# Optimization experiments

Measured on AMD Instinct MI355X. Metric: run time of the kernel, lower is better.

Reference implementation:

```python
import jax, jax.numpy as jnp
import numpy as np

B, D, E, K, H = 4096, 1024, 8, 2, 8  # batch, dim, num_experts, top_k, num_heads


def setup_inputs() -> dict:
    key = jax.random.key(0)
    ks = jax.random.split(key, 6)
    w = lambda k, shape: jax.random.normal(k, shape, jnp.float32) * 0.02
    return dict(
        x=jax.random.normal(ks[0], (B, D), jnp.float32),
        y=jax.random.normal(ks[1], (B, D), jnp.float32),
        Wqkv=w(ks[2], (E, D, 3 * D)),      # per-expert qkv weight (no bias)
        Wg=w(ks[3], (D, E)),               # gating weight
        bg=jnp.zeros((E,), jnp.float32),   # gating bias
        Wp=w(ks[4], (D, D)),               # output proj weight
        bp=jnp.zeros((D,), jnp.float32),   # output proj bias
        expert_bias=jnp.zeros((E,), jnp.float32),  # non-trainable load-balance bias
    )


def reference(x, y, Wqkv, Wg, bg, Wp, bp, expert_bias):
    Bn, Dn = x.shape
    hd = Dn // H
    scale = hd ** -0.5

    # gating: softmax then add (non-trainable) expert bias, then top-k
    gate = jax.nn.softmax(x @ Wg + bg, axis=-1) + expert_bias          # [B,E]
    vals, idx = jax.lax.top_k(gate, K)                                  # [B,K]
    # combine top-k gate values into a per-expert weight vector (indices distinct)
    g = jnp.sum(jax.nn.one_hot(idx, E, dtype=x.dtype) * vals[..., None], axis=1)  # [B,E]

    # dense per-expert qkv projections, then gate-weighted combine
    qkv_x = jnp.einsum('be,beh->bh', g, jnp.einsum('bd,edh->beh', x, Wqkv))  # [B,3D]
    qkv_y = jnp.einsum('be,beh->bh', g, jnp.einsum('bd,edh->beh', y, Wqkv))  # [B,3D]

    qkv_x = qkv_x.reshape(Bn, 3, H, hd)
    qkv_y = qkv_y.reshape(Bn, 3, H, hd)
    q = qkv_y[:, 0]   # [B,H,hd] (query from y)
    k = qkv_x[:, 1]   # [B,H,hd]
    v = qkv_x[:, 2]   # [B,H,hd]

    # attention across the heads axis (heads act as the sequence here)
    attn = jax.nn.softmax(jnp.einsum('bid,bjd->bij', q, k) * scale, axis=-1)  # [B,H,H]
    out = jnp.einsum('bij,bjd->bid', attn, v)                                 # [B,H,hd]
    # torch: .transpose(1,2).reshape(B,N) -> flatten as (hd, H)
    out = jnp.swapaxes(out, 1, 2).reshape(Bn, Dn)
    return out @ Wp + bp
```

## Files before the change

### kernel.cpp

```cpp
#include <hip/hip_runtime.h>
#include <cstdint>
#include <cstddef>

#define B_TOK 4096
#define D_DIM 1024
#define E_NUM 8
#define N3    3072

typedef float f32x4 __attribute__((ext_vector_type(4)));
typedef __bf16 bf16x8 __attribute__((ext_vector_type(8)));

__device__ __forceinline__ unsigned short f2bf(float f) {
  unsigned u = __float_as_uint(f);
  u += 0x7fffu + ((u >> 16) & 1u);
  return (unsigned short)(u >> 16);
}
__device__ __forceinline__ float bf_lo(unsigned u) { return __uint_as_float(u << 16); }
__device__ __forceinline__ float bf_hi(unsigned u) { return __uint_as_float(u & 0xffff0000u); }

__device__ __forceinline__ void stage16(const unsigned short* g, unsigned short* lds) {
  __builtin_amdgcn_global_load_lds(
      (const __attribute__((address_space(1))) void*)(uintptr_t)(const void*)g,
      (__attribute__((address_space(3))) void*)(uintptr_t)(void*)lds,
      16, 0, 0);
}

#define PREP_B   B_TOK
#define TQ_B     (16 * 48 * 8)
#define TP_B     (16 * 16)
#define FUSED_B  (PREP_B + TQ_B + TP_B)

__global__ __launch_bounds__(256)
void fused_prep_kernel(const float* __restrict__ x, const float* __restrict__ y,
                       const float* __restrict__ Wg, const float* __restrict__ bg,
                       const float* __restrict__ ebias,
                       const float* __restrict__ Wqkv, const float* __restrict__ Wp,
                       unsigned short* __restrict__ xb, unsigned short* __restrict__ yb,
                       unsigned short* __restrict__ wqkvT, unsigned short* __restrict__ wpT,
                       int* __restrict__ tok_expert, float* __restrict__ tok_weight)
{
  __shared__ float tile[64][65];
  __shared__ float red[4][E_NUM];
  const int t = threadIdx.x;
  const int grp = blockIdx.x / 41;
  const int pos = blockIdx.x % 41;

  if (pos < 16) {
    const int b = grp * 16 + pos;
    const int w = t >> 6, l = t & 63;
    float4 xv = *(const float4*)(x + (size_t)b * D_DIM + 4 * t);
    float4 yv = *(const float4*)(y + (size_t)b * D_DIM + 4 * t);
    ushort4 px; px.x = f2bf(xv.x); px.y = f2bf(xv.y); px.z = f2bf(xv.z); px.w = f2bf(xv.w);
    *(ushort4*)(xb + (size_t)b * D_DIM + 4 * t) = px;
    ushort4 py; py.x = f2bf(yv.x); py.y = f2bf(yv.y); py.z = f2bf(yv.z); py.w = f2bf(yv.w);
    *(ushort4*)(yb + (size_t)b * D_DIM + 4 * t) = py;

    float a[E_NUM];
#pragma unroll
    for (int e = 0; e < E_NUM; ++e) a[e] = 0.f;
    const float xa[4] = {xv.x, xv.y, xv.z, xv.w};
#pragma unroll
    for (int j = 0; j < 4; ++j) {
      const float4* wr4 = (const float4*)(Wg + (size_t)(4 * t + j) * E_NUM);
      float4 w0 = wr4[0], w1 = wr4[1];
      a[0] += xa[j] * w0.x; a[1] += xa[j] * w0.y;
      a[2] += xa[j] * w0.z; a[3] += xa[j] * w0.w;
      a[4] += xa[j] * w1.x; a[5] += xa[j] * w1.y;
      a[6] += xa[j] * w1.z; a[7] += xa[j] * w1.w;
    }

    float s0, s1, s2, s3;
    {
      const bool b0 = (l & 1);
      float r0_ = __shfl_xor(b0 ? a[0] : a[4], 1);
      float r1_ = __shfl_xor(b0 ? a[1] : a[5], 1);
      float r2_ = __shfl_xor(b0 ? a[2] : a[6], 1);
      float r3_ = __shfl_xor(b0 ? a[3] : a[7], 1);
      s0 = (b0 ? a[4] : a[0]) + r0_;
      s1 = (b0 ? a[5] : a[1]) + r1_;
      s2 = (b0 ? a[6] : a[2]) + r2_;
      s3 = (b0 ? a[7] : a[3]) + r3_;
    }
    float u0, u1;
    {
      const bool b1 = (l & 2);
      float r0_ = __shfl_xor(b1 ? s0 : s2, 2);
      float r1_ = __shfl_xor(b1 ? s1 : s3, 2);
      u0 = (b1 ? s2 : s0) + r0_;
      u1 = (b1 ? s3 : s1) + r1_;
    }
    float v_;
    {
      const bool b2 = (l & 4);
      float r0_ = __shfl_xor(b2 ? u0 : u1, 4);
      v_ = (b2 ? u1 : u0) + r0_;
    }
    v_ += __shfl_xor(v_, 8);
    v_ += __shfl_xor(v_, 16);
    v_ += __shfl_xor(v_, 32);
    if (l < 8) {
      const int e = ((l & 1) << 2) | (l & 2) | ((l >> 2) & 1);
      red[w][e] = v_;
    }
    __syncthreads();
    if (t == 0) {
      float logit[E_NUM];
#pragma unroll
      for (int e = 0; e < E_NUM; ++e)
        logit[e] = red[0][e] + red[1][e] + red[2][e] + red[3][e] + bg[e];
      float m = logit[0];
#pragma unroll
      for (int e = 1; e < E_NUM; ++e) m = fmaxf(m, logit[e]);
      float p[E_NUM], s = 0.f;
#pragma unroll
      for (int e = 0; e < E_NUM; ++e) { p[e] = expf(logit[e] - m); s += p[e]; }
      float inv = 1.f / s;
      float gate[E_NUM];
#pragma unroll
      for (int e = 0; e < E_NUM; ++e) gate[e] = p[e] * inv + ebias[e];
      int i1 = 0; float v1 = gate[0];
#pragma unroll
      for (int e = 1; e < E_NUM; ++e) if (gate[e] > v1) { v1 = gate[e]; i1 = e; }
      int i2 = -1; float v2 = -1e30f;
#pragma unroll
      for (int e = 0; e < E_NUM; ++e) if (e != i1 && gate[e] > v2) { v2 = gate[e]; i2 = e; }
      tok_expert[b * 2] = i1; tok_expert[b * 2 + 1] = i2;
      tok_weight[b * 2] = v1; tok_weight[b * 2 + 1] = v2;
    }
    return;
  }

  const int tid2 = grp * 25 + (pos - 16);
  const float* in; unsigned short* outp; int R, C, r0, c0; size_t mo;
  if (tid2 < TQ_B) {
    int id = tid2;
    int rt = id & 15; int rest = id >> 4;
    int ct = rest % 48; int mz = rest / 48;
    in = Wqkv; outp = wqkvT; R = 1024; C = 3072;
    r0 = rt * 64; c0 = ct * 64; mo = (size_t)mz * R * C;
  } else {
    int id = tid2 - TQ_B;
    int rt = id & 15; int ct = id >> 4;
    in = Wp; outp = wpT; R = 1024; C = 1024;
    r0 = rt * 64; c0 = ct * 64; mo = 0;
  }
  const int tq = t & 15;
  const int tr = t >> 4;
  {
    const float* src = in + mo + (size_t)(r0 + tr) * C + (c0 + 4 * tq);
    float4 v0 = *(const float4*)(src);
    float4 v1 = *(const float4*)(src + (size_t)16 * C);
    float4 v2 = *(const float4*)(src + (size_t)32 * C);
    float4 v3 = *(const float4*)(src + (size_t)48 * C);
    tile[tr][4 * tq] = v0.x;      tile[tr][4 * tq + 1] = v0.y;
    tile[tr][4 * tq + 2] = v0.z;  tile[tr][4 * tq + 3] = v0.w;
    tile[tr + 16][4 * tq] = v1.x;     tile[tr + 16][4 * tq + 1] = v1.y;
    tile[tr + 16][4 * tq + 2] = v1.z; tile[tr + 16][4 * tq + 3] = v1.w;
    tile[tr + 32][4 * tq] = v2.x;     tile[tr + 32][4 * tq + 1] = v2.y;
    tile[tr + 32][4 * tq + 2] = v2.z; tile[tr + 32][4 * tq + 3] = v2.w;
    tile[tr + 48][4 * tq] = v3.x;     tile[tr + 48][4 * tq + 1] = v3.y;
    tile[tr + 48][4 * tq + 2] = v3.z; tile[tr + 48][4 * tq + 3] = v3.w;
  }
  __syncthreads();
  {
    const int rw = 4 * tq;
#pragma unroll
    for (int p = 0; p < 4; ++p) {
      const int c = tr + 16 * p;
      float a0 = tile[rw][c], a1 = tile[rw + 1][c];
      float a2 = tile[rw + 2][c], a3 = tile[rw + 3][c];
      ushort4 o;
      o.x = f2bf(a0); o.y = f2bf(a1); o.z = f2bf(a2); o.w = f2bf(a3);
      *(ushort4*)(outp + mo + (size_t)(c0 + c) * R + (r0 + rw)) = o;
    }
  }
}

#define NT_ENT (B_TOK * 2)
#define ENT_PER_T (NT_ENT / 256)
__global__ __launch_bounds__(256)
void route_kernel(const int* __restrict__ tok_expert, const float* __restrict__ tok_weight,
                  int* __restrict__ eoff, int* __restrict__ slot_token,
                  float* __restrict__ slot_weight, int* __restrict__ tok_slot)
{
  __shared__ int cnt[256][E_NUM];
  __shared__ int sub[E_NUM][8];
  __shared__ int tot[E_NUM];
  __shared__ int eoff_s[E_NUM];
  const int t = threadIdx.x;

  {
    int h[E_NUM];
#pragma unroll
    for (int e = 0; e < E_NUM; ++e) h[e] = 0;
    for (int p = 0; p < ENT_PER_T; ++p) {
      int e = tok_expert[t * ENT_PER_T + p];
      h[e]++;
    }
#pragma unroll
    for (int e = 0; e < E_NUM; ++e) cnt[t][e] = h[e];
  }
  __syncthreads();

  if (t < 64) {
    int e = t & 7, g = t >> 3;
    int run = 0;
    for (int i = g * 32; i < (g + 1) * 32; ++i) {
      int v = cnt[i][e];
      cnt[i][e] = run;
      run += v;
    }
    sub[e][g] = run;
  }
  __syncthreads();
  if (t < E_NUM) {
    int run = 0;
#pragma unroll
    for (int g = 0; g < 8; ++g) {
      int v = sub[t][g];
      sub[t][g] = run;
      run += v;
    }
    tot[t] = run;
  }
  __syncthreads();
  if (t < 64) {
    int e = t & 7, g = t >> 3;
    int basev = sub[e][g];
    for (int i = g * 32; i < (g + 1) * 32; ++i) cnt[i][e] += basev;
  }
  if (t == 0) {
    int a = 0;
#pragma unroll
    for (int e = 0; e < E_NUM; ++e) { eoff_s[e] = a; eoff[e] = a; a += tot[e]; }
    eoff[E_NUM] = a;
  }
  __syncthreads();

  for (int p = 0; p < ENT_PER_T; ++p) {
    int i = t * ENT_PER_T + p;
    int e = tok_expert[i];
    int sl = eoff_s[e] + cnt[t][e];
    cnt[t][e] = cnt[t][e] + 1;
    slot_token[sl] = i >> 1;
    slot_weight[sl] = tok_weight[i];
    tok_slot[i] = sl;
  }
}

#define MOE_NWG 6144
#define MOE_CPX (MOE_NWG / 8)
__global__ __launch_bounds__(256, 4)
void moe_gemm_kernel(const unsigned short* __restrict__ yb, const unsigned short* __restrict__ xb,
                     const unsigned short* __restrict__ wqkvT,
                     unsigned short* __restrict__ qkvslot,
                     const int* __restrict__ slot_token, const float* __restrict__ slot_weight,
                     const int* __restrict__ eoff)
{
  __shared__ __align__(16) unsigned short As[128 * 64];
  __shared__ __align__(16) unsigned short Bs[128 * 64];

  const int id = blockIdx.x;
  const int swz = (id & 7) * MOE_CPX + (id >> 3);
  const int nt = swz % 24;
  const int mtE = swz / 24;
  const int mt = mtE & 31;
  const int e  = mtE >> 5;

  const int tid = threadIdx.x;
  const int w = tid >> 6, l = tid & 63;
  const int base = eoff[e], cnt = eoff[e + 1] - base;
  if (mt * 128 >= cnt) return;
  const int slot_base = base + mt * 128;
  const int valid = min(128, cnt - mt * 128);
  const int nc = nt * 128;

  const unsigned short* Abase = (nt < 8) ? yb : xb;
  const unsigned short* Bbase = wqkvT + ((size_t)e * N3 + nc) * D_DIM;

  const int csw = (((l & 7) ^ (l >> 3)) << 3);
  const unsigned short* aptr[4];
  const unsigned short* bptr[4];
#pragma unroll
  for (int i = 0; i < 4; ++i) {
    int r = (w * 4 + i) * 8 + (l >> 3);
    int rA = r < valid ? r : (valid - 1);
    int t = slot_token[slot_base + rA];
    aptr[i] = Abase + (size_t)t * D_DIM + csw;
    bptr[i] = Bbase + (size_t)r * D_DIM + csw;
  }

  f32x4 acc[4][4];
#pragma unroll
  for (int mi = 0; mi < 4; ++mi)
#pragma unroll
    for (int ni = 0; ni < 4; ++ni) acc[mi][ni] = (f32x4){0.f, 0.f, 0.f, 0.f};

  const int wr = w >> 1, wc = w & 1;
  const int arow = wr * 64 + (l & 15);
  const int brow = wc * 64 + (l & 15);

  for (int kt = 0; kt < 16; ++kt) {
    __syncthreads();
#pragma unroll
    for (int i = 0; i < 4; ++i) {
      stage16(aptr[i] + kt * 64, &As[(w * 4 + i) * 512]);
      stage16(bptr[i] + kt * 64, &Bs[(w * 4 + i) * 512]);
    }
    __syncthreads();
#pragma unroll
    for (int ks = 0; ks < 2; ++ks) {
      const int eoffk = (((ks * 4 + (l >> 4)) ^ (l & 7)) << 3);
      bf16x8 af[4], bfv[4];
#pragma unroll
      for (int mi = 0; mi < 4; ++mi)
        af[mi] = *(const bf16x8*)&As[(arow + mi * 16) * 64 + eoffk];
#pragma unroll
      for (int ni = 0; ni < 4; ++ni)
        bfv[ni] = *(const bf16x8*)&Bs[(brow + ni * 16) * 64 + eoffk];
#pragma unroll
      for (int mi = 0; mi < 4; ++mi)
#pragma unroll
        for (int ni = 0; ni < 4; ++ni)
          acc[mi][ni] = __builtin_amdgcn_mfma_f32_16x16x32_bf16(af[mi], bfv[ni], acc[mi][ni], 0, 0, 0);
    }
  }

  const int crow0 = wr * 64 + ((l >> 4) << 2);
  const int ccol = wc * 64 + (l & 15);
#pragma unroll
  for (int mi = 0; mi < 4; ++mi) {
#pragma unroll
    for (int j = 0; j < 4; ++j) {
      int rloc = crow0 + mi * 16 + j;
      if (rloc < valid) {
        int sl = slot_base + rloc;
        float wgt = slot_weight[sl];
        size_t ro = (size_t)sl * N3 + nc + ccol;
#pragma unroll
        for (int ni = 0; ni < 4; ++ni)
          qkvslot[ro + ni * 16] = f2bf(acc[mi][ni][j] * wgt);
      }
    }
  }
}

__global__ __launch_bounds__(256)
void attn_kernel(const unsigned short* __restrict__ qkvslot,
                 const int* __restrict__ tok_slot,
                 unsigned short* __restrict__ attno)
{
  __shared__ unsigned short obuf[4][1024];
  const int w = threadIdx.x >> 6, l = threadIdx.x & 63;
  const int b0 = blockIdx.x * 4;
  const int b = b0 + w;
  const int s0 = tok_slot[b * 2], s1 = tok_slot[b * 2 + 1];
  const unsigned* p0 = (const unsigned*)(qkvslot + (size_t)s0 * N3);
  const unsigned* p1 = (const unsigned*)(qkvslot + (size_t)s1 * N3);

  float q[8][2], k[8][2], v[8][2];
#pragma unroll
  for (int i = 0; i < 8; ++i) {
    unsigned a0 = p0[i * 64 + l],        a1 = p1[i * 64 + l];
    unsigned b0v = p0[512 + i * 64 + l], b1v = p1[512 + i * 64 + l];
    unsigned c0 = p0[1024 + i * 64 + l], c1 = p1[1024 + i * 64 + l];
    q[i][0] = bf_lo(a0) + bf_lo(a1); q[i][1] = bf_hi(a0) + bf_hi(a1);
    k[i][0] = bf_lo(b0v) + bf_lo(b1v); k[i][1] = bf_hi(b0v) + bf_hi(b1v);
    v[i][0] = bf_lo(c0) + bf_lo(c1); v[i][1] = bf_hi(c0) + bf_hi(c1);
  }

  float S[8][8];
#pragma unroll
  for (int i = 0; i < 8; ++i)
#pragma unroll
    for (int j = 0; j < 8; ++j)
      S[i][j] = q[i][0] * k[j][0] + q[i][1] * k[j][1];

#pragma unroll
  for (int off = 32; off; off >>= 1)
#pragma unroll
    for (int i = 0; i < 8; ++i)
#pragma unroll
      for (int j = 0; j < 8; ++j)
        S[i][j] += __shfl_xor(S[i][j], off);

  const float scale = 0.08838834764831843f;
#pragma unroll
  for (int i = 0; i < 8; ++i) {
    float m = S[i][0];
#pragma unroll
    for (int j = 1; j < 8; ++j) m = fmaxf(m, S[i][j]);
    float P[8], sum = 0.f;
#pragma unroll
    for (int j = 0; j < 8; ++j) { P[j] = expf((S[i][j] - m) * scale); sum += P[j]; }
    float inv = 1.f / sum;
    float o0 = 0.f, o1 = 0.f;
#pragma unroll
    for (int j = 0; j < 8; ++j) { o0 += P[j] * v[j][0]; o1 += P[j] * v[j][1]; }
    obuf[w][(2 * l) * 8 + i]     = f2bf(o0 * inv);
    obuf[w][(2 * l + 1) * 8 + i] = f2bf(o1 * inv);
  }
  __syncthreads();
  const int t = threadIdx.x;
#pragma unroll
  for (int p = 0; p < 4; ++p) {
    int j = t + 256 * p;
    int tk = j >> 8, c = j & 255;
    *(ushort4*)(attno + (size_t)(b0 + tk) * D_DIM + 4 * c) = *(ushort4*)&obuf[tk][4 * c];
  }
}

__global__ __launch_bounds__(256, 4)
void final_gemm_kernel(const unsigned short* __restrict__ attno,
                       const unsigned short* __restrict__ wpT,
                       const float* __restrict__ bp,
                       float* __restrict__ out)
{
  __shared__ __align__(16) unsigned short As[64 * 64];
  __shared__ __align__(16) unsigned short Bs[128 * 64];

  const int tid = threadIdx.x;
  const int w = tid >> 6, l = tid & 63;
  const int nt = blockIdx.x, mt = blockIdx.y;

  const int csw = (((l & 7) ^ (l >> 3)) << 3);
  const unsigned short* aptr[2];
  const unsigned short* bptr[4];
#pragma unroll
  for (int i = 0; i < 2; ++i) {
    int r = (w * 2 + i) * 8 + (l >> 3);
    aptr[i] = attno + (size_t)(mt * 64 + r) * D_DIM + csw;
  }
#pragma unroll
  for (int i = 0; i < 4; ++i) {
    int r = (w * 4 + i) * 8 + (l >> 3);
    bptr[i] = wpT + (size_t)(nt * 128 + r) * D_DIM + csw;
  }

  f32x4 acc[2][4];
#pragma unroll
  for (int mi = 0; mi < 2; ++mi)
#pragma unroll
    for (int ni = 0; ni < 4; ++ni) acc[mi][ni] = (f32x4){0.f, 0.f, 0.f, 0.f};

  const int wr = w >> 1, wc = w & 1;
  const int arow = wr * 32 + (l & 15);
  const int brow = wc * 64 + (l & 15);

  for (int kt = 0; kt < 16; ++kt) {
    __syncthreads();
#pragma unroll
    for (int i = 0; i < 2; ++i)
      stage16(aptr[i] + kt * 64, &As[(w * 2 + i) * 512]);
#pragma unroll
    for (int i = 0; i < 4; ++i)
      stage16(bptr[i] + kt * 64, &Bs[(w * 4 + i) * 512]);
    __syncthreads();
#pragma unroll
    for (int ks = 0; ks < 2; ++ks) {
      const int eoffk = (((ks * 4 + (l >> 4)) ^ (l & 7)) << 3);
      bf16x8 af[2], bfv[4];
#pragma unroll
      for (int mi = 0; mi < 2; ++mi)
        af[mi] = *(const bf16x8*)&As[(arow + mi * 16) * 64 + eoffk];
#pragma unroll
      for (int ni = 0; ni < 4; ++ni)
        bfv[ni] = *(const bf16x8*)&Bs[(brow + ni * 16) * 64 + eoffk];
#pragma unroll
      for (int mi = 0; mi < 2; ++mi)
#pragma unroll
        for (int ni = 0; ni < 4; ++ni)
          acc[mi][ni] = __builtin_amdgcn_mfma_f32_16x16x32_bf16(af[mi], bfv[ni], acc[mi][ni], 0, 0, 0);
    }
  }

  const int crow0 = wr * 32 + ((l >> 4) << 2);
  const int ccol = wc * 64 + (l & 15);
#pragma unroll
  for (int mi = 0; mi < 2; ++mi) {
#pragma unroll
    for (int j = 0; j < 4; ++j) {
      int rg = mt * 64 + crow0 + mi * 16 + j;
#pragma unroll
      for (int ni = 0; ni < 4; ++ni) {
        int cg = nt * 128 + ccol + ni * 16;
        out[(size_t)rg * D_DIM + cg] = acc[mi][ni][j] + bp[cg];
      }
    }
  }
}

extern "C" void kernel_launch(void* const* d_in, const int* in_sizes, int n_in,
                              void* d_out, int out_size, void* d_ws, size_t ws_size,
                              hipStream_t stream)
{
  const float* x     = (const float*)d_in[0];
  const float* y     = (const float*)d_in[1];
  const float* Wqkv  = (const float*)d_in[2];
  const float* Wg    = (const float*)d_in[3];
  const float* bg    = (const float*)d_in[4];
  const float* Wp    = (const float*)d_in[5];
  const float* bp    = (const float*)d_in[6];
  const float* ebias = (const float*)d_in[7];
  float* out = (float*)d_out;

  char* ws = (char*)d_ws;
  size_t off_b = 0;
  auto take = [&](size_t bytes) -> char* {
    char* p = ws + off_b;
    off_b += (bytes + 255) & ~(size_t)255;
    return p;
  };
  unsigned short* xb       = (unsigned short*)take((size_t)B_TOK * D_DIM * 2);
  unsigned short* yb       = (unsigned short*)take((size_t)B_TOK * D_DIM * 2);
  unsigned short* wqkvT    = (unsigned short*)take((size_t)E_NUM * N3 * D_DIM * 2);
  unsigned short* wpT      = (unsigned short*)take((size_t)D_DIM * D_DIM * 2);
  unsigned short* qkvslot  = (unsigned short*)take((size_t)B_TOK * 2 * N3 * 2);
  unsigned short* attno    = (unsigned short*)take((size_t)B_TOK * D_DIM * 2);
  int*   eoff        = (int*)take(16 * 4);
  int*   tok_expert  = (int*)take((size_t)B_TOK * 2 * 4);
  float* tok_weight  = (float*)take((size_t)B_TOK * 2 * 4);
  int*   tok_slot    = (int*)take((size_t)B_TOK * 2 * 4);
  int*   slot_token  = (int*)take((size_t)B_TOK * 2 * 4);
  float* slot_weight = (float*)take((size_t)B_TOK * 2 * 4);

  if (ws_size < off_b) return;

  fused_prep_kernel<<<FUSED_B, 256, 0, stream>>>(x, y, Wg, bg, ebias, Wqkv, Wp,
                                                 xb, yb, wqkvT, wpT, tok_expert, tok_weight);
  route_kernel<<<1, 256, 0, stream>>>(tok_expert, tok_weight, eoff, slot_token,
                                      slot_weight, tok_slot);
  moe_gemm_kernel<<<MOE_NWG, 256, 0, stream>>>(yb, xb, wqkvT, qkvslot,
                                               slot_token, slot_weight, eoff);
  attn_kernel<<<B_TOK / 4, 256, 0, stream>>>(qkvslot, tok_slot, attno);
  final_gemm_kernel<<<dim3(8, 64), 256, 0, stream>>>(attno, wpT, bp, out);
}
```

Measured before the change: 161.5 us.

## Fold routing into prep kernel via last-block counter and compact MoE tile grid

Removes the separate single-block route kernel by having the last finishing gating block (tracked by an atomic done-counter) perform the expert histogram, prefix sum and slot scatter inside the prep kernel. That block also emits a compact list of valid (expert, m-tile) pairs, so the MoE GEMM launches 24*71 workgroups instead of 6144, most of which previously exited immediately. This saves one launch and the cost of scheduling many empty workgroups. In exchange it adds a memset launch, an atomic plus threadfence in every gating block, and a serialized tail in the last block.

```diff
diff --git a/kernel.cpp b/kernel.cpp
--- a/kernel.cpp
+++ b/kernel.cpp
@@ -29,6 +29,9 @@
 #define TQ_B     (16 * 48 * 8)
 #define TP_B     (16 * 16)
 #define FUSED_B  (PREP_B + TQ_B + TP_B)
+
+#define NT_ENT (B_TOK * 2)
+#define ENT_PER_T (NT_ENT / 256)
 
 __global__ __launch_bounds__(256)
 void fused_prep_kernel(const float* __restrict__ x, const float* __restrict__ y,
@@ -37,10 +40,20 @@
                        const float* __restrict__ Wqkv, const float* __restrict__ Wp,
                        unsigned short* __restrict__ xb, unsigned short* __restrict__ yb,
                        unsigned short* __restrict__ wqkvT, unsigned short* __restrict__ wpT,
-                       int* __restrict__ tok_expert, float* __restrict__ tok_weight)
+                       int* __restrict__ tok_expert, float* __restrict__ tok_weight,
+                       int* __restrict__ done_ctr,
+                       int* __restrict__ eoff, int* __restrict__ slot_token,
+                       float* __restrict__ slot_weight, int* __restrict__ tok_slot,
+                       int* __restrict__ tile_list, int* __restrict__ n_tiles)
 {
   __shared__ float tile[64][65];
   __shared__ float red[4][E_NUM];
+  __shared__ int last_s;
+  int (*rcnt)[E_NUM] = (int (*)[E_NUM])&tile[0][0];
+  int (*rsub)[8]     = (int (*)[8])((char*)&tile[0][0] + 8192);
+  int* rtot          = (int*)((char*)&tile[0][0] + 8448);
+  int* reoff         = (int*)((char*)&tile[0][0] + 8480);
+
   const int t = threadIdx.x;
   const int grp = blockIdx.x / 41;
   const int pos = blockIdx.x % 41;
@@ -126,6 +139,74 @@
       for (int e = 0; e < E_NUM; ++e) if (e != i1 && gate[e] > v2) { v2 = gate[e]; i2 = e; }
       tok_expert[b * 2] = i1; tok_expert[b * 2 + 1] = i2;
       tok_weight[b * 2] = v1; tok_weight[b * 2 + 1] = v2;
+      __threadfence();
+      int old = atomicAdd(done_ctr, 1);
+      last_s = (old == PREP_B - 1);
+    }
+    __syncthreads();
+    if (!last_s) return;
+    __threadfence();
+
+    {
+      int h[E_NUM];
+#pragma unroll
+      for (int e = 0; e < E_NUM; ++e) h[e] = 0;
+      for (int p = 0; p < ENT_PER_T; ++p) {
+        int e = tok_expert[t * ENT_PER_T + p];
+        h[e]++;
+      }
+#pragma unroll
+      for (int e = 0; e < E_NUM; ++e) rcnt[t][e] = h[e];
+    }
+    __syncthreads();
+    if (t < 64) {
+      int e = t & 7, g = t >> 3;
+      int run = 0;
+      for (int i = g * 32; i < (g + 1) * 32; ++i) {
+        int v = rcnt[i][e];
+        rcnt[i][e] = run;
+        run += v;
+      }
+      rsub[e][g] = run;
+    }
+    __syncthreads();
+    if (t < E_NUM) {
+      int run = 0;
+#pragma unroll
+      for (int g = 0; g < 8; ++g) {
+        int v = rsub[t][g];
+        rsub[t][g] = run;
+        run += v;
+      }
+      rtot[t] = run;
+    }
+    __syncthreads();
+    if (t < 64) {
+      int e = t & 7, g = t >> 3;
+      int basev = rsub[e][g];
+      for (int i = g * 32; i < (g + 1) * 32; ++i) rcnt[i][e] += basev;
+    }
+    if (t == 0) {
+      int a = 0, n = 0;
+#pragma unroll
+      for (int e = 0; e < E_NUM; ++e) {
+        reoff[e] = a; eoff[e] = a;
+        int c = rtot[e];
+        for (int j = 0; j * 128 < c; ++j) tile_list[n++] = e | (j << 8);
+        a += c;
+      }
+      eoff[E_NUM] = a;
+      n_tiles[0] = n;
+    }
+    __syncthreads();
+    for (int p = 0; p < ENT_PER_T; ++p) {
+      int i = t * ENT_PER_T + p;
+      int e = tok_expert[i];
+      int sl = reoff[e] + rcnt[t][e];
+      rcnt[t][e] = rcnt[t][e] + 1;
+      slot_token[sl] = i >> 1;
+      slot_weight[sl] = tok_weight[i];
+      tok_slot[i] = sl;
     }
     return;
   }
@@ -176,101 +257,32 @@
   }
 }
 
-#define NT_ENT (B_TOK * 2)
-#define ENT_PER_T (NT_ENT / 256)
-__global__ __launch_bounds__(256)
-void route_kernel(const int* __restrict__ tok_expert, const float* __restrict__ tok_weight,
-                  int* __restrict__ eoff, int* __restrict__ slot_token,
-                  float* __restrict__ slot_weight, int* __restrict__ tok_slot)
-{
-  __shared__ int cnt[256][E_NUM];
-  __shared__ int sub[E_NUM][8];
-  __shared__ int tot[E_NUM];
-  __shared__ int eoff_s[E_NUM];
-  const int t = threadIdx.x;
-
-  {
-    int h[E_NUM];
-#pragma unroll
-    for (int e = 0; e < E_NUM; ++e) h[e] = 0;
-    for (int p = 0; p < ENT_PER_T; ++p) {
-      int e = tok_expert[t * ENT_PER_T + p];
-      h[e]++;
-    }
-#pragma unroll
-    for (int e = 0; e < E_NUM; ++e) cnt[t][e] = h[e];
-  }
-  __syncthreads();
-
-  if (t < 64) {
-    int e = t & 7, g = t >> 3;
-    int run = 0;
-    for (int i = g * 32; i < (g + 1) * 32; ++i) {
-      int v = cnt[i][e];
-      cnt[i][e] = run;
-      run += v;
-    }
-    sub[e][g] = run;
-  }
-  __syncthreads();
-  if (t < E_NUM) {
-    int run = 0;
-#pragma unroll
-    for (int g = 0; g < 8; ++g) {
-      int v = sub[t][g];
-      sub[t][g] = run;
-      run += v;
-    }
-    tot[t] = run;
-  }
-  __syncthreads();
-  if (t < 64) {
-    int e = t & 7, g = t >> 3;
-    int basev = sub[e][g];
-    for (int i = g * 32; i < (g + 1) * 32; ++i) cnt[i][e] += basev;
-  }
-  if (t == 0) {
-    int a = 0;
-#pragma unroll
-    for (int e = 0; e < E_NUM; ++e) { eoff_s[e] = a; eoff[e] = a; a += tot[e]; }
-    eoff[E_NUM] = a;
-  }
-  __syncthreads();
-
-  for (int p = 0; p < ENT_PER_T; ++p) {
-    int i = t * ENT_PER_T + p;
-    int e = tok_expert[i];
-    int sl = eoff_s[e] + cnt[t][e];
-    cnt[t][e] = cnt[t][e] + 1;
-    slot_token[sl] = i >> 1;
-    slot_weight[sl] = tok_weight[i];
-    tok_slot[i] = sl;
-  }
-}
-
-#define MOE_NWG 6144
-#define MOE_CPX (MOE_NWG / 8)
+#define MOE_MAXT 71
+#define MOE_NWG  (24 * MOE_MAXT)
+#define MOE_CPX  (MOE_NWG / 8)
 __global__ __launch_bounds__(256, 4)
 void moe_gemm_kernel(const unsigned short* __restrict__ yb, const unsigned short* __restrict__ xb,
                      const unsigned short* __restrict__ wqkvT,
                      unsigned short* __restrict__ qkvslot,
                      const int* __restrict__ slot_token, const float* __restrict__ slot_weight,
-                     const int* __restrict__ eoff)
+                     const int* __restrict__ eoff,
+                     const int* __restrict__ tile_list, const int* __restrict__ n_tiles)
 {
   __shared__ __align__(16) unsigned short As[128 * 64];
   __shared__ __align__(16) unsigned short Bs[128 * 64];
 
   const int id = blockIdx.x;
   const int swz = (id & 7) * MOE_CPX + (id >> 3);
-  const int nt = swz % 24;
-  const int mtE = swz / 24;
-  const int mt = mtE & 31;
-  const int e  = mtE >> 5;
+  const int tix = swz / 24;
+  const int nt  = swz % 24;
+  if (tix >= n_tiles[0]) return;
+  const int packed = tile_list[tix];
+  const int e  = packed & 255;
+  const int mt = packed >> 8;
 
   const int tid = threadIdx.x;
   const int w = tid >> 6, l = tid & 63;
   const int base = eoff[e], cnt = eoff[e + 1] - base;
-  if (mt * 128 >= cnt) return;
   const int slot_base = base + mt * 128;
   const int valid = min(128, cnt - mt * 128);
   const int nc = nt * 128;
@@ -523,15 +535,21 @@
   int*   tok_slot    = (int*)take((size_t)B_TOK * 2 * 4);
   int*   slot_token  = (int*)take((size_t)B_TOK * 2 * 4);
   float* slot_weight = (float*)take((size_t)B_TOK * 2 * 4);
+  int*   done_ctr    = (int*)take(4);
+  int*   tile_list   = (int*)take(MOE_MAXT * 4);
+  int*   n_tiles     = (int*)take(4);
 
   if (ws_size < off_b) return;
 
+  hipMemsetAsync(done_ctr, 0, 4, stream);
+
   fused_prep_kernel<<<FUSED_B, 256, 0, stream>>>(x, y, Wg, bg, ebias, Wqkv, Wp,
-                                                 xb, yb, wqkvT, wpT, tok_expert, tok_weight);
-  route_kernel<<<1, 256, 0, stream>>>(tok_expert, tok_weight, eoff, slot_token,
-                                      slot_weight, tok_slot);
+                                                 xb, yb, wqkvT, wpT, tok_expert, tok_weight,
+                                                 done_ctr, eoff, slot_token, slot_weight,
+                                                 tok_slot, tile_list, n_tiles);
   moe_gemm_kernel<<<MOE_NWG, 256, 0, stream>>>(yb, xb, wqkvT, qkvslot,
-                                               slot_token, slot_weight, eoff);
+                                               slot_token, slot_weight, eoff,
+                                               tile_list, n_tiles);
   attn_kernel<<<B_TOK / 4, 256, 0, stream>>>(qkvslot, tok_slot, attno);
   final_gemm_kernel<<<dim3(8, 64), 256, 0, stream>>>(attno, wpT, bp, out);
 }
```

Result: slower. 366.6 us (+127.1%).

## Double-buffer LDS staging in MoE GEMM with prefetch two K-tiles ahead

Applied to the files above, without the earlier changes.

Switches the MoE GEMM's A and B shared-memory tiles to two buffers and prefetches two K-steps ahead with global_load_lds, waiting with explicit vmcnt counts instead of full syncthreads. This lets global-to-LDS loads overlap the MFMA work rather than stalling each iteration. LDS use doubles to 64KB per block, which may cut occupancy below the launch-bounds target of 4 blocks. The hand-written waitcnt values also depend on the exact number of outstanding loads.

```diff
diff --git a/kernel.cpp b/kernel.cpp
--- a/kernel.cpp
+++ b/kernel.cpp
@@ -257,8 +257,8 @@
                      const int* __restrict__ slot_token, const float* __restrict__ slot_weight,
                      const int* __restrict__ eoff)
 {
-  __shared__ __align__(16) unsigned short As[128 * 64];
-  __shared__ __align__(16) unsigned short Bs[128 * 64];
+  __shared__ __align__(16) unsigned short As[2][128 * 64];
+  __shared__ __align__(16) unsigned short Bs[2][128 * 64];
 
   const int id = blockIdx.x;
   const int swz = (id & 7) * MOE_CPX + (id >> 3);
@@ -300,29 +300,50 @@
   const int arow = wr * 64 + (l & 15);
   const int brow = wc * 64 + (l & 15);
 
+#pragma unroll
+  for (int i = 0; i < 4; ++i) {
+    stage16(aptr[i], &As[0][(w * 4 + i) * 512]);
+    stage16(bptr[i], &Bs[0][(w * 4 + i) * 512]);
+  }
+#pragma unroll
+  for (int i = 0; i < 4; ++i) {
+    stage16(aptr[i] + 64, &As[1][(w * 4 + i) * 512]);
+    stage16(bptr[i] + 64, &Bs[1][(w * 4 + i) * 512]);
+  }
+
   for (int kt = 0; kt < 16; ++kt) {
-    __syncthreads();
-#pragma unroll
-    for (int i = 0; i < 4; ++i) {
-      stage16(aptr[i] + kt * 64, &As[(w * 4 + i) * 512]);
-      stage16(bptr[i] + kt * 64, &Bs[(w * 4 + i) * 512]);
-    }
-    __syncthreads();
+    if (kt < 15) asm volatile("s_waitcnt vmcnt(8)" ::: "memory");
+    else         asm volatile("s_waitcnt vmcnt(0)" ::: "memory");
+    __builtin_amdgcn_s_barrier();
+    __builtin_amdgcn_sched_barrier(0);
+
+    const unsigned short* Asc = As[kt & 1];
+    const unsigned short* Bsc = Bs[kt & 1];
 #pragma unroll
     for (int ks = 0; ks < 2; ++ks) {
       const int eoffk = (((ks * 4 + (l >> 4)) ^ (l & 7)) << 3);
       bf16x8 af[4], bfv[4];
 #pragma unroll
       for (int mi = 0; mi < 4; ++mi)
-        af[mi] = *(const bf16x8*)&As[(arow + mi * 16) * 64 + eoffk];
+        af[mi] = *(const bf16x8*)&Asc[(arow + mi * 16) * 64 + eoffk];
 #pragma unroll
       for (int ni = 0; ni < 4; ++ni)
-        bfv[ni] = *(const bf16x8*)&Bs[(brow + ni * 16) * 64 + eoffk];
+        bfv[ni] = *(const bf16x8*)&Bsc[(brow + ni * 16) * 64 + eoffk];
 #pragma unroll
       for (int mi = 0; mi < 4; ++mi)
 #pragma unroll
         for (int ni = 0; ni < 4; ++ni)
           acc[mi][ni] = __builtin_amdgcn_mfma_f32_16x16x32_bf16(af[mi], bfv[ni], acc[mi][ni], 0, 0, 0);
+    }
+
+    __builtin_amdgcn_sched_barrier(0);
+    __builtin_amdgcn_s_barrier();
+    if (kt + 2 < 16) {
+#pragma unroll
+      for (int i = 0; i < 4; ++i) {
+        stage16(aptr[i] + (kt + 2) * 64, &As[kt & 1][(w * 4 + i) * 512]);
+        stage16(bptr[i] + (kt + 2) * 64, &Bs[kt & 1][(w * 4 + i) * 512]);
+      }
     }
   }
 
```

New measurement: 172.9 us. +7.1%, slower.
